# Kernel optimization log

Hardware: AMD Instinct MI355X
Metric: run time of the kernel (lower is better)

## Reference

```python
import jax, jax.numpy as jnp
import numpy as np

B, S, E, H, W, G = 1, 2048, 1024, 16, 512, 16
HD = E // H

def setup_inputs() -> dict:
    key = jax.random.key(0)
    ks = jax.random.split(key, 12)
    s = 1.0 / np.sqrt(E)
    inp = {
        'query': jax.random.normal(ks[0], (B, S, E), jnp.float32),
        'key':   jax.random.normal(ks[1], (B, S, E), jnp.float32),
        'value': jax.random.normal(ks[2], (B, S, E), jnp.float32),
        'is_global': jnp.broadcast_to(jnp.arange(S) < G, (B, S)),
        'Wq': jax.random.uniform(ks[3], (E, E), jnp.float32, -s, s),
        'bq': jax.random.uniform(ks[4], (E,),   jnp.float32, -s, s),
        'Wk': jax.random.uniform(ks[5], (E, E), jnp.float32, -s, s),
        'bk': jax.random.uniform(ks[6], (E,),   jnp.float32, -s, s),
        'Wv': jax.random.uniform(ks[7], (E, E), jnp.float32, -s, s),
        'bv': jax.random.uniform(ks[8], (E,),   jnp.float32, -s, s),
        'Wo': jax.random.uniform(ks[9], (E, E), jnp.float32, -s, s),
        'bo': jax.random.uniform(ks[10], (E,),  jnp.float32, -s, s),
    }
    return inp

def reference(query, key, value, is_global, Wq, bq, Wk, bk, Wv, bv, Wo, bo):
    # Linear projections (torch Linear: x @ W.T + b), reshape to [B,H,S,HD]
    def proj(x, Wt, b):
        return (x @ Wt.T + b).reshape(B, S, H, HD).transpose(0, 2, 1, 3)
    q = proj(query, Wq, bq)
    k = proj(key,   Wk, bk)
    v = proj(value, Wv, bv)

    scores = jnp.einsum('bhqd,bhkd->bhqk', q, k) / np.sqrt(HD)  # [B,H,S,S]

    idx = jnp.arange(S)
    window_mask = jnp.abs(idx[None, :] - idx[:, None]) <= W      # [S,S]
    combined = (window_mask[None, None]
                | is_global[:, None, None, :]    # global keys
                | is_global[:, None, :, None])   # global queries
    scores = jnp.where(combined, scores, -jnp.inf)

    attn = jax.nn.softmax(scores, axis=-1)  # dropout is identity in eval
    out = jnp.einsum('bhqk,bhkd->bhqd', attn, v)
    out = out.transpose(0, 2, 1, 3).reshape(B, S, E)
    return out @ Wo.T + bo
```

## Files before the change

kernel.cpp:

```cpp
#include <hip/hip_runtime.h>
#include <hip/hip_bf16.h>
#include <stdint.h>

#define S_LEN 2048
#define E_DIM 1024
#define N_HEAD 16
#define HD 64
#define WIN 512

typedef __attribute__((ext_vector_type(4))) float f32x4;
typedef __attribute__((ext_vector_type(8))) short bf16x8;
typedef __attribute__((ext_vector_type(8))) unsigned short u16x8;

__device__ __forceinline__ unsigned f2bf2(float lo, float hi) {
  __hip_bfloat162 h = __float22bfloat162_rn(make_float2(lo, hi));
  return *reinterpret_cast<unsigned*>(&h);
}
__device__ __forceinline__ unsigned short f2bf(float f) {
  __hip_bfloat16 h = __float2bfloat16(f);
  return *reinterpret_cast<unsigned short*>(&h);
}
__device__ __forceinline__ float bf2f(unsigned short u) {
  union { unsigned u; float f; } v; v.u = (unsigned)u << 16; return v.f;
}

__device__ __forceinline__ void gl2lds16(const void* g, void* l) {
  __builtin_amdgcn_global_load_lds((const __attribute__((address_space(1))) void*)g,
                                   (__attribute__((address_space(3))) void*)l, 16, 0, 0);
}

__global__ __launch_bounds__(256) void convert_kernel(
    const float* __restrict__ q, const float* __restrict__ k, const float* __restrict__ v,
    const float* __restrict__ wq, const float* __restrict__ wk,
    const float* __restrict__ wv, const float* __restrict__ wo,
    unsigned short* __restrict__ dst, const int* __restrict__ gm,
    unsigned char* __restrict__ kmask, unsigned char* __restrict__ bflag) {
  const size_t SE = (size_t)S_LEN * E_DIM, EE = (size_t)E_DIM * E_DIM;
  if (blockIdx.x == 0) {
    __shared__ int badw;
    int tid = threadIdx.x;
    if (tid == 0) badw = 0;
    __syncthreads();
    for (int i = tid; i < S_LEN / 4; i += 256) {
      int vv = gm[i];
      if (vv != 0 && vv != 1) atomicOr(&badw, 1);
    }
    __syncthreads();
    const int bytes = badw;
    const unsigned char* gb = (const unsigned char*)gm;
    for (int i = tid; i < S_LEN; i += 256)
      kmask[i] = bytes ? (unsigned char)(gb[i] != 0) : (unsigned char)(gm[i] != 0);
    if (tid < S_LEN / 64) {
      unsigned char any = 0;
      for (int j = 0; j < 64; ++j) {
        int i = tid * 64 + j;
        any |= bytes ? (unsigned char)(gb[i] != 0) : (unsigned char)(gm[i] != 0);
      }
      bflag[tid] = any;
    }
  }
  size_t i = ((size_t)blockIdx.x * 256 + threadIdx.x) * 8;
  const float* src;
  size_t off;
  if (i < SE) { src = q; off = i; }
  else if (i < 2 * SE) { src = k; off = i - SE; }
  else if (i < 3 * SE) { src = v; off = i - 2 * SE; }
  else if (i < 3 * SE + EE) { src = wq; off = i - 3 * SE; }
  else if (i < 3 * SE + 2 * EE) { src = wk; off = i - 3 * SE - EE; }
  else if (i < 3 * SE + 3 * EE) { src = wv; off = i - 3 * SE - 2 * EE; }
  else { src = wo; off = i - 3 * SE - 3 * EE; }
  f32x4 x0 = *(const f32x4*)(src + off);
  f32x4 x1 = *(const f32x4*)(src + off + 4);
  union { u16x8 v; unsigned u[4]; } o;
  o.u[0] = f2bf2(x0[0], x0[1]); o.u[1] = f2bf2(x0[2], x0[3]);
  o.u[2] = f2bf2(x1[0], x1[1]); o.u[3] = f2bf2(x1[2], x1[3]);
  *(u16x8*)(dst + i) = o.v;
}

template <int BN, int OUTMODE>
__device__ __forceinline__ void gemm_body(const unsigned short* __restrict__ A,
                                          const unsigned short* __restrict__ B,
                                          const float* __restrict__ bias,
                                          void* __restrict__ Out_) {
  __shared__ unsigned short As[64][64];
  __shared__ unsigned short Bs[BN][64];
  constexpr int MI = (BN == 128) ? 2 : 1;
  const int tid = threadIdx.x;
  const int wid = tid >> 6, lane = tid & 63;
  const int a = lane & 15, g = lane >> 4;
  const int m0 = blockIdx.y * 64, n0 = blockIdx.x * BN;
  const int wr = (BN == 128) ? (wid >> 1) * 32 : wid * 16;
  const int wc = (BN == 128) ? (wid & 1) * 64 : 0;
  const int l8 = lane >> 3, l7 = (lane & 7) * 8;
  f32x4 acc[MI][4] = {};

  for (int k0 = 0; k0 < E_DIM; k0 += 64) {
    __syncthreads();
#pragma unroll
    for (int c = 0; c < 2; ++c) {
      const int r0 = (wid * 2 + c) * 8;
      gl2lds16(A + (size_t)(m0 + r0 + l8) * E_DIM + k0 + l7, &As[r0][0]);
    }
#pragma unroll
    for (int c = 0; c < BN / 32; ++c) {
      const int r0 = (wid * (BN / 32) + c) * 8;
      gl2lds16(B + (size_t)(n0 + r0 + l8) * E_DIM + k0 + l7, &Bs[r0][0]);
    }
    __syncthreads();
#pragma unroll
    for (int s = 0; s < 2; ++s) {
      bf16x8 af[MI], bfv[4];
#pragma unroll
      for (int i = 0; i < MI; ++i) af[i] = *(const bf16x8*)&As[wr + i * 16 + a][s * 32 + g * 8];
#pragma unroll
      for (int j = 0; j < 4; ++j) bfv[j] = *(const bf16x8*)&Bs[wc + j * 16 + a][s * 32 + g * 8];
#pragma unroll
      for (int i = 0; i < MI; ++i)
#pragma unroll
        for (int j = 0; j < 4; ++j)
          acc[i][j] = __builtin_amdgcn_mfma_f32_16x16x32_bf16(af[i], bfv[j], acc[i][j], 0, 0, 0);
    }
  }
#pragma unroll
  for (int i = 0; i < MI; ++i)
#pragma unroll
    for (int j = 0; j < 4; ++j) {
      const int row0 = m0 + wr + i * 16 + g * 4;
      const int col = n0 + wc + j * 16 + a;
      if (OUTMODE == 2) {
        unsigned short* O = (unsigned short*)Out_;
        unsigned lo = f2bf2(acc[i][j][0] + bias[col], acc[i][j][1] + bias[col]);
        unsigned hi = f2bf2(acc[i][j][2] + bias[col], acc[i][j][3] + bias[col]);
        uint2 pk; pk.x = lo; pk.y = hi;
        *(uint2*)&O[(size_t)col * S_LEN + row0] = pk;
      } else {
#pragma unroll
        for (int r = 0; r < 4; ++r) {
          float v = acc[i][j][r] + bias[col];
          if (OUTMODE == 0) {
            unsigned short* O = (unsigned short*)Out_;
            O[((size_t)(col >> 6) * S_LEN + row0 + r) * HD + (col & 63)] = f2bf(v);
          } else {
            float* O = (float*)Out_;
            O[(size_t)(row0 + r) * E_DIM + col] = v;
          }
        }
      }
    }
}

__global__ __launch_bounds__(256) void gemm_qkv_kernel(
    const unsigned short* __restrict__ wsbf, const float* __restrict__ bq,
    const float* __restrict__ bk, const float* __restrict__ bv,
    unsigned short* __restrict__ Qo, unsigned short* __restrict__ Ko,
    unsigned short* __restrict__ Vo) {
  const size_t SE = (size_t)S_LEN * E_DIM, EE = (size_t)E_DIM * E_DIM;
  const int z = blockIdx.z;
  const unsigned short* A = wsbf + (size_t)z * SE;
  const unsigned short* W = wsbf + 3 * SE + (size_t)z * EE;
  const float* b = z == 0 ? bq : (z == 1 ? bk : bv);
  if (z == 2)
    gemm_body<128, 2>(A, W, b, Vo);
  else
    gemm_body<128, 0>(A, W, b, z == 0 ? Qo : Ko);
}

__global__ __launch_bounds__(256) void gemm_out_kernel(
    const unsigned short* __restrict__ Oi, const unsigned short* __restrict__ Wo,
    const float* __restrict__ bo, float* __restrict__ out) {
  gemm_body<64, 1>(Oi, Wo, bo, out);
}

__global__ __launch_bounds__(256) void attn_kernel(
    const unsigned short* __restrict__ Q, const unsigned short* __restrict__ K,
    const unsigned short* __restrict__ Vt_g, const unsigned char* __restrict__ kmask,
    const unsigned char* __restrict__ bflag, unsigned short* __restrict__ O,
    unsigned short* __restrict__ PA, float2* __restrict__ ML) {
  __shared__ unsigned short Kt[128][72];
  __shared__ unsigned short Vt[64][136];
  __shared__ float Plf[4][16][132];
  __shared__ unsigned char kmAll[S_LEN];

  const int tid = threadIdx.x;
  const int wid = tid >> 6, lane = tid & 63;
  const int a = lane & 15, g = lane >> 4;

  if (blockIdx.x >= 32) {
    const int h = blockIdx.y;
    const int split = (blockIdx.x - 32) * 4 + wid;
    const int k0 = split * 64;
    const unsigned short* Kh = K + (size_t)h * S_LEN * HD;
    const unsigned short* Vh = Vt_g + (size_t)h * HD * S_LEN;
    const float c = 0.18033688011112042f;

    const size_t qb = ((size_t)h * S_LEN + a) * HD;
    const bf16x8 qf0 = *(const bf16x8*)(Q + qb + g * 8);
    const bf16x8 qf1 = *(const bf16x8*)(Q + qb + 32 + g * 8);

    f32x4 s4[4];
#pragma unroll
    for (int t = 0; t < 4; ++t) {
      const unsigned short* kp = Kh + (size_t)(k0 + t * 16 + a) * HD;
      bf16x8 kf0 = *(const bf16x8*)(kp + g * 8);
      bf16x8 kf1 = *(const bf16x8*)(kp + 32 + g * 8);
      f32x4 z = {0.f, 0.f, 0.f, 0.f};
      z = __builtin_amdgcn_mfma_f32_16x16x32_bf16(qf0, kf0, z, 0, 0, 0);
      z = __builtin_amdgcn_mfma_f32_16x16x32_bf16(qf1, kf1, z, 0, 0, 0);
      s4[t] = z;
    }
    float m[4], l[4], tv[4][4];
#pragma unroll
    for (int t = 0; t < 4; ++t)
#pragma unroll
      for (int r = 0; r < 4; ++r) tv[t][r] = s4[t][r] * c;
#pragma unroll
    for (int r = 0; r < 4; ++r) {
      float tm = fmaxf(fmaxf(tv[0][r], tv[1][r]), fmaxf(tv[2][r], tv[3][r]));
#pragma unroll
      for (int off = 1; off < 16; off <<= 1) tm = fmaxf(tm, __shfl_xor(tm, off, 16));
      float ps = 0.f;
#pragma unroll
      for (int t = 0; t < 4; ++t) {
        float p = __builtin_amdgcn_exp2f(tv[t][r] - tm);
        tv[t][r] = p; ps += p;
      }
#pragma unroll
      for (int off = 1; off < 16; off <<= 1) ps += __shfl_xor(ps, off, 16);
      m[r] = tm; l[r] = ps;
    }
#pragma unroll
    for (int t = 0; t < 4; ++t)
#pragma unroll
      for (int r = 0; r < 4; ++r)
        Plf[wid][g * 4 + r][t * 16 + a] = tv[t][r];
    bf16x8 pa[2];
#pragma unroll
    for (int ks = 0; ks < 2; ++ks) {
      const float* pp = &Plf[wid][a][ks * 32 + g * 8];
      f32x4 x0 = *(const f32x4*)pp, x1 = *(const f32x4*)(pp + 4);
      union { bf16x8 v; unsigned u[4]; } pu;
      pu.u[0] = f2bf2(x0[0], x0[1]); pu.u[1] = f2bf2(x0[2], x0[3]);
      pu.u[2] = f2bf2(x1[0], x1[1]); pu.u[3] = f2bf2(x1[2], x1[3]);
      pa[ks] = pu.v;
    }
    f32x4 acc[4] = {};
#pragma unroll
    for (int d = 0; d < 4; ++d)
#pragma unroll
      for (int ks = 0; ks < 2; ++ks) {
        bf16x8 vf = *(const bf16x8*)(Vh + (size_t)(d * 16 + a) * S_LEN + k0 + ks * 32 + g * 8);
        acc[d] = __builtin_amdgcn_mfma_f32_16x16x32_bf16(pa[ks], vf, acc[d], 0, 0, 0);
      }
    unsigned short* pacc = PA + (((size_t)h * 32 + split) * 16) * 64;
#pragma unroll
    for (int d = 0; d < 4; ++d)
#pragma unroll
      for (int r = 0; r < 4; ++r)
        pacc[(g * 4 + r) * 64 + d * 16 + a] = f2bf(acc[d][r]);
    if (a == 0) {
      float2* pml = ML + ((size_t)h * 32 + split) * 16;
#pragma unroll
      for (int r = 0; r < 4; ++r) pml[g * 4 + r] = make_float2(m[r], l[r]);
    }
    return;
  }

  const int fid = blockIdx.x + (blockIdx.y << 5);
  const int logical = ((fid & 7) << 6) + (fid >> 3);
  const int h = logical >> 5;
  const int q0 = (logical & 31) << 6;
  const int qw = q0 + wid * 16;

  ((uint2*)kmAll)[tid] = ((const uint2*)kmask)[tid];

  const size_t qbase = ((size_t)h * S_LEN + (qw + a)) * HD;
  const bf16x8 qf0 = *(const bf16x8*)(Q + qbase + g * 8);
  const bf16x8 qf1 = *(const bf16x8*)(Q + qbase + 32 + g * 8);

  __syncthreads();
  int qg[4];
#pragma unroll
  for (int r = 0; r < 4; ++r) qg[r] = kmAll[qw + g * 4 + r];

  unsigned amask = 0;
  {
    int lo = (q0 - WIN) >> 7; if (lo < 0) lo = 0;
    int hi = (q0 + 63 + WIN) >> 7; if (hi > 15) hi = 15;
#pragma unroll
    for (int t2 = 0; t2 < 16; ++t2) {
      bool act = (t2 >= lo && t2 <= hi) || bflag[2 * t2] || bflag[2 * t2 + 1];
      amask |= (unsigned)act << t2;
    }
  }

  float m[4], l[4];
  f32x4 acc[4];
#pragma unroll
  for (int r = 0; r < 4; ++r) { m[r] = -1e30f; l[r] = 0.f; }
#pragma unroll
  for (int d = 0; d < 4; ++d) acc[d] = f32x4{0.f, 0.f, 0.f, 0.f};

  const unsigned short* Kh = K + (size_t)h * S_LEN * HD;
  const unsigned short* Vh = Vt_g + (size_t)h * HD * S_LEN;
  const float c = 0.18033688011112042f;

  u16x8 kreg[4], vreg[4];
  auto issue = [&](int k0) {
    const u16x8* pk = (const u16x8*)(Kh + (size_t)(k0 + (tid >> 1)) * HD + (tid & 1) * 32);
    kreg[0] = pk[0]; kreg[1] = pk[1]; kreg[2] = pk[2]; kreg[3] = pk[3];
    const u16x8* pv = (const u16x8*)(Vh + (size_t)(tid >> 2) * S_LEN + k0 + (tid & 3) * 32);
    vreg[0] = pv[0]; vreg[1] = pv[1]; vreg[2] = pv[2]; vreg[3] = pv[3];
  };

  int kb = amask ? __builtin_ctz(amask) : 16;
  if (kb < 16) issue(kb * 128);
  while (kb < 16) {
    const unsigned rem = amask >> (kb + 1);
    const int nxt = rem ? kb + 1 + __builtin_ctz(rem) : 16;
    const int k0 = kb * 128;

    __syncthreads();
    {
      u16x8* dk = (u16x8*)&Kt[tid >> 1][(tid & 1) * 32];
      dk[0] = kreg[0]; dk[1] = kreg[1]; dk[2] = kreg[2]; dk[3] = kreg[3];
      u16x8* dv = (u16x8*)&Vt[tid >> 2][(tid & 3) * 32];
      dv[0] = vreg[0]; dv[1] = vreg[1]; dv[2] = vreg[2]; dv[3] = vreg[3];
    }
    __syncthreads();
    if (nxt < 16) issue(nxt * 128);

    f32x4 s4[8];
    __builtin_amdgcn_s_setprio(1);
#pragma unroll
    for (int t = 0; t < 8; ++t) {
      bf16x8 kf0 = *(const bf16x8*)&Kt[t * 16 + a][g * 8];
      bf16x8 kf1 = *(const bf16x8*)&Kt[t * 16 + a][32 + g * 8];
      f32x4 z = {0.f, 0.f, 0.f, 0.f};
      z = __builtin_amdgcn_mfma_f32_16x16x32_bf16(qf0, kf0, z, 0, 0, 0);
      z = __builtin_amdgcn_mfma_f32_16x16x32_bf16(qf1, kf1, z, 0, 0, 0);
      s4[t] = z;
    }
    __builtin_amdgcn_s_setprio(0);

    float tv[8][4];
    const bool interior = (k0 >= q0 - 449) && (k0 <= q0 + 385);
    if (interior) {
#pragma unroll
      for (int t = 0; t < 8; ++t)
#pragma unroll
        for (int r = 0; r < 4; ++r) tv[t][r] = s4[t][r] * c;
    } else {
#pragma unroll
      for (int t = 0; t < 8; ++t) {
        const int kc = k0 + t * 16 + a;
        const int kglob = kmAll[kc];
#pragma unroll
        for (int r = 0; r < 4; ++r) {
          const int qr = qw + g * 4 + r;
          bool inc = qg[r] || kglob || ((unsigned)(qr - kc + WIN) <= (unsigned)(2 * WIN));
          tv[t][r] = inc ? s4[t][r] * c : -3.0e38f;
        }
      }
    }

#pragma unroll
    for (int r = 0; r < 4; ++r) {
      float tm = fmaxf(fmaxf(tv[0][r], tv[1][r]), fmaxf(tv[2][r], tv[3][r]));
      tm = fmaxf(tm, fmaxf(fmaxf(tv[4][r], tv[5][r]), fmaxf(tv[6][r], tv[7][r])));
#pragma unroll
      for (int off = 1; off < 16; off <<= 1) tm = fmaxf(tm, __shfl_xor(tm, off, 16));
      const float mn = fmaxf(m[r], tm);
      const float rs = __builtin_amdgcn_exp2f(m[r] - mn);
      m[r] = mn;
      float ps = 0.f;
#pragma unroll
      for (int t = 0; t < 8; ++t) {
        float p = __builtin_amdgcn_exp2f(tv[t][r] - mn);
        tv[t][r] = p; ps += p;
      }
#pragma unroll
      for (int off = 1; off < 16; off <<= 1) ps += __shfl_xor(ps, off, 16);
      l[r] = l[r] * rs + ps;
#pragma unroll
      for (int d = 0; d < 4; ++d) acc[d][r] *= rs;
    }

#pragma unroll
    for (int t = 0; t < 8; ++t)
#pragma unroll
      for (int r = 0; r < 4; ++r)
        Plf[wid][g * 4 + r][t * 16 + a] = tv[t][r];
    bf16x8 pa[4];
#pragma unroll
    for (int ks = 0; ks < 4; ++ks) {
      const float* pp = &Plf[wid][a][ks * 32 + g * 8];
      f32x4 x0 = *(const f32x4*)pp, x1 = *(const f32x4*)(pp + 4);
      union { bf16x8 v; unsigned u[4]; } pu;
      pu.u[0] = f2bf2(x0[0], x0[1]); pu.u[1] = f2bf2(x0[2], x0[3]);
      pu.u[2] = f2bf2(x1[0], x1[1]); pu.u[3] = f2bf2(x1[2], x1[3]);
      pa[ks] = pu.v;
    }

    __builtin_amdgcn_s_setprio(1);
#pragma unroll
    for (int d = 0; d < 4; ++d)
#pragma unroll
      for (int ks = 0; ks < 4; ++ks) {
        bf16x8 vf = *(const bf16x8*)&Vt[d * 16 + a][ks * 32 + g * 8];
        acc[d] = __builtin_amdgcn_mfma_f32_16x16x32_bf16(pa[ks], vf, acc[d], 0, 0, 0);
      }
    __builtin_amdgcn_s_setprio(0);
    kb = nxt;
  }

#pragma unroll
  for (int d = 0; d < 4; ++d)
#pragma unroll
    for (int r = 0; r < 4; ++r) {
      const int qr = qw + g * 4 + r;
      float v = acc[d][r] / l[r];
      O[(size_t)qr * E_DIM + h * HD + d * 16 + a] = f2bf(v);
    }
}

__global__ __launch_bounds__(256) void combine_glb_kernel(
    const unsigned short* __restrict__ PA, const float2* __restrict__ ML,
    unsigned short* __restrict__ O) {
  const int h = blockIdx.x, tid = threadIdx.x;
  const int row = tid >> 4, d0 = (tid & 15) * 4;
  float M = -1e30f;
#pragma unroll 8
  for (int s = 0; s < 32; ++s) M = fmaxf(M, ML[((size_t)h * 32 + s) * 16 + row].x);
  float L = 0.f, o0 = 0.f, o1 = 0.f, o2 = 0.f, o3 = 0.f;
  for (int s = 0; s < 32; ++s) {
    float2 ml = ML[((size_t)h * 32 + s) * 16 + row];
    float w = __builtin_amdgcn_exp2f(ml.x - M);
    L += w * ml.y;
    const unsigned short* p = PA + (((size_t)h * 32 + s) * 16 + row) * 64 + d0;
    o0 += w * bf2f(p[0]); o1 += w * bf2f(p[1]);
    o2 += w * bf2f(p[2]); o3 += w * bf2f(p[3]);
  }
  const float inv = 1.0f / L;
  uint2 pk;
  pk.x = f2bf2(o0 * inv, o1 * inv);
  pk.y = f2bf2(o2 * inv, o3 * inv);
  *(uint2*)&O[(size_t)row * E_DIM + h * HD + d0] = pk;
}

extern "C" void kernel_launch(void* const* d_in, const int* in_sizes, int n_in,
                              void* d_out, int out_size, void* d_ws, size_t ws_size,
                              hipStream_t stream) {
  const float* q  = (const float*)d_in[0];
  const float* k  = (const float*)d_in[1];
  const float* v  = (const float*)d_in[2];
  const int* isg  = (const int*)d_in[3];
  const float* Wq = (const float*)d_in[4];
  const float* bq = (const float*)d_in[5];
  const float* Wk = (const float*)d_in[6];
  const float* bk = (const float*)d_in[7];
  const float* Wv = (const float*)d_in[8];
  const float* bv = (const float*)d_in[9];
  const float* Wo = (const float*)d_in[10];
  const float* bo = (const float*)d_in[11];

  const size_t SE = (size_t)S_LEN * E_DIM, EE = (size_t)E_DIM * E_DIM;
  unsigned short* wsbf = (unsigned short*)d_ws;
  unsigned short* Qb = wsbf + 3 * SE + 4 * EE;
  unsigned short* Kb = Qb + SE;
  unsigned short* Vb = Kb + SE;
  unsigned short* Ob = wsbf;
  unsigned char* kmask = (unsigned char*)(Vb + SE);
  unsigned char* bflag = kmask + S_LEN;
  unsigned short* PA = wsbf + SE;
  float2* ML = (float2*)(PA + (size_t)16 * 32 * 16 * 64);

  const int total_conv_blocks = (int)((3 * SE + 4 * EE) / (256 * 8));
  convert_kernel<<<total_conv_blocks, 256, 0, stream>>>(q, k, v, Wq, Wk, Wv, Wo, wsbf,
                                                        isg, kmask, bflag);
  gemm_qkv_kernel<<<dim3(E_DIM / 128, S_LEN / 64, 3), 256, 0, stream>>>(
      wsbf, bq, bk, bv, Qb, Kb, Vb);
  attn_kernel<<<dim3(40, N_HEAD), 256, 0, stream>>>(Qb, Kb, Vb, kmask, bflag, Ob, PA, ML);
  combine_glb_kernel<<<N_HEAD, 256, 0, stream>>>(PA, ML, Ob);
  gemm_out_kernel<<<dim3(E_DIM / 64, S_LEN / 64), 256, 0, stream>>>(
      Ob, wsbf + 3 * SE + 3 * EE, bo, (float*)d_out);
}
```

Baseline: 117.6 us.

## Register-prefetch next GEMM tile and pad LDS rows to avoid bank conflicts

Replaces direct global-to-LDS loads in the projection GEMM with loads into registers. The next k-tile's loads are issued right after the barrier, so they overlap with the MFMA work on the current tile. LDS rows are padded from 64 to 72 elements to reduce bank conflicts on the fragment reads. This costs extra VGPRs for the staging registers and extra LDS, which may lower occupancy.

After: 119.2 us. Within noise of the previous version (+1.3%).

```diff
diff --git a/kernel.cpp b/kernel.cpp
--- a/kernel.cpp
+++ b/kernel.cpp
@@ -22,11 +22,6 @@
 }
 __device__ __forceinline__ float bf2f(unsigned short u) {
   union { unsigned u; float f; } v; v.u = (unsigned)u << 16; return v.f;
-}
-
-__device__ __forceinline__ void gl2lds16(const void* g, void* l) {
-  __builtin_amdgcn_global_load_lds((const __attribute__((address_space(1))) void*)g,
-                                   (__attribute__((address_space(3))) void*)l, 16, 0, 0);
 }
 
 __global__ __launch_bounds__(256) void convert_kernel(
@@ -82,8 +77,8 @@
                                           const unsigned short* __restrict__ B,
                                           const float* __restrict__ bias,
                                           void* __restrict__ Out_) {
-  __shared__ unsigned short As[64][64];
-  __shared__ unsigned short Bs[BN][64];
+  __shared__ unsigned short As[64][72];
+  __shared__ unsigned short Bs[BN][72];
   constexpr int MI = (BN == 128) ? 2 : 1;
   const int tid = threadIdx.x;
   const int wid = tid >> 6, lane = tid & 63;
@@ -91,22 +86,39 @@
   const int m0 = blockIdx.y * 64, n0 = blockIdx.x * BN;
   const int wr = (BN == 128) ? (wid >> 1) * 32 : wid * 16;
   const int wc = (BN == 128) ? (wid & 1) * 64 : 0;
-  const int l8 = lane >> 3, l7 = (lane & 7) * 8;
+  const int arow = tid >> 2, acol = (tid & 3) * 16;
   f32x4 acc[MI][4] = {};
 
+  u16x8 areg[2], breg[4];
+  auto issue = [&](int k0) {
+    const u16x8* pa = (const u16x8*)(A + (size_t)(m0 + arow) * E_DIM + k0 + acol);
+    areg[0] = pa[0]; areg[1] = pa[1];
+    if (BN == 128) {
+      const u16x8* pb = (const u16x8*)(B + (size_t)(n0 + (tid >> 1)) * E_DIM + k0 + (tid & 1) * 32);
+      breg[0] = pb[0]; breg[1] = pb[1]; breg[2] = pb[2]; breg[3] = pb[3];
+    } else {
+      const u16x8* pb = (const u16x8*)(B + (size_t)(n0 + arow) * E_DIM + k0 + acol);
+      breg[0] = pb[0]; breg[1] = pb[1];
+    }
+  };
+
+  issue(0);
   for (int k0 = 0; k0 < E_DIM; k0 += 64) {
     __syncthreads();
-#pragma unroll
-    for (int c = 0; c < 2; ++c) {
-      const int r0 = (wid * 2 + c) * 8;
-      gl2lds16(A + (size_t)(m0 + r0 + l8) * E_DIM + k0 + l7, &As[r0][0]);
-    }
-#pragma unroll
-    for (int c = 0; c < BN / 32; ++c) {
-      const int r0 = (wid * (BN / 32) + c) * 8;
-      gl2lds16(B + (size_t)(n0 + r0 + l8) * E_DIM + k0 + l7, &Bs[r0][0]);
-    }
-    __syncthreads();
+    {
+      *(u16x8*)&As[arow][acol] = areg[0];
+      *(u16x8*)&As[arow][acol + 8] = areg[1];
+      if (BN == 128) {
+        u16x8* db = (u16x8*)&Bs[tid >> 1][(tid & 1) * 32];
+        db[0] = breg[0]; db[1] = breg[1]; db[2] = breg[2]; db[3] = breg[3];
+      } else {
+        *(u16x8*)&Bs[arow][acol] = breg[0];
+        *(u16x8*)&Bs[arow][acol + 8] = breg[1];
+      }
+    }
+    __syncthreads();
+    if (k0 + 64 < E_DIM) issue(k0 + 64);
+
 #pragma unroll
     for (int s = 0; s < 2; ++s) {
       bf16x8 af[MI], bfv[4];
```
